# Performance work log

Measured on AMD Instinct MI355X. Metric: run time of the kernel, lower is better.

## Reference

```python
import jax, jax.numpy as jnp
import numpy as np

N = 100000   # nodes
F = 256      # input features
H = 64       # hidden dims
C = 40       # classes
L = 4        # GGNN layers
E = 1200000  # edges


def setup_inputs() -> dict:
    key = jax.random.key(0)
    ks = jax.random.split(key, 8)
    x = jax.random.normal(ks[0], (N, F), dtype=jnp.float32)
    edge_index = jax.random.randint(ks[1], (2, E), 0, N, dtype=jnp.int64)
    # glorot-initialized projection weights
    weight_in = jax.random.uniform(ks[2], (F, H), jnp.float32, -1.0, 1.0) * np.sqrt(6.0 / (F + H))
    weight_out = jax.random.uniform(ks[3], (H, C), jnp.float32, -1.0, 1.0) * np.sqrt(6.0 / (H + C))
    # GatedGraphConv: per-layer message weight [L, H, H], shared GRUCell params
    conv_weight = jax.random.uniform(ks[4], (L, H, H), jnp.float32, -1.0, 1.0) * np.sqrt(6.0 / (2 * H))
    s = 1.0 / np.sqrt(H)
    w_ih = jax.random.uniform(ks[5], (3 * H, H), jnp.float32, -s, s)
    w_hh = jax.random.uniform(ks[6], (3 * H, H), jnp.float32, -s, s)
    b_ih = jax.random.uniform(ks[7], (3 * H,), jnp.float32, -s, s)
    b_hh = jnp.zeros((3 * H,), jnp.float32)
    return {"x": x, "edge_index": edge_index, "weight_in": weight_in,
            "weight_out": weight_out, "conv_weight": conv_weight,
            "w_ih": w_ih, "w_hh": w_hh, "b_ih": b_ih, "b_hh": b_hh}


def _gru_cell(a, h, w_ih, w_hh, b_ih, b_hh):
    # torch.nn.GRUCell math: input a, hidden h
    gi = a @ w_ih.T + b_ih
    gh = h @ w_hh.T + b_hh
    i_r, i_z, i_n = jnp.split(gi, 3, axis=1)
    h_r, h_z, h_n = jnp.split(gh, 3, axis=1)
    r = jax.nn.sigmoid(i_r + h_r)
    z = jax.nn.sigmoid(i_z + h_z)
    n = jnp.tanh(i_n + r * h_n)
    return (1.0 - z) * n + z * h


def reference(x, edge_index, weight_in, weight_out, conv_weight, w_ih, w_hh, b_ih, b_hh):
    n_nodes = x.shape[0]
    src, dst = edge_index[0], edge_index[1]
    h = x @ weight_in  # [N, H]
    for i in range(conv_weight.shape[0]):
        m = h @ conv_weight[i]                                   # [N, H]
        agg = jax.ops.segment_sum(m[src], dst, num_segments=n_nodes)  # scatter-add
        h = _gru_cell(agg, h, w_ih, w_hh, b_ih, b_hh)
    out = h @ weight_out  # [N, C]
    return jax.nn.log_softmax(out, axis=1)
```

## Files before the change

kernel.cpp:

```cpp
#include <hip/hip_runtime.h>


#define DEVI __device__ __forceinline__

typedef __attribute__((ext_vector_type(8))) short short8;
typedef __attribute__((ext_vector_type(4))) short bf16x4;
typedef __attribute__((ext_vector_type(4))) float f32x4;

constexpr int N_NODES   = 100000;
constexpr int F_IN      = 256;
constexpr int H_DIM     = 64;
constexpr int C_OUT     = 40;
constexpr int ROW_TILES = N_NODES / 16;
constexpr int CH        = 8192;
constexpr int NBUCK     = (N_NODES + 127) / 128;
constexpr int LB_STRIDE = NBUCK + 1;
constexpr int BCAP      = 2048;

DEVI float bf2f(unsigned short u) {
    unsigned v = ((unsigned)u) << 16;
    float f; __builtin_memcpy(&f, &v, 4); return f;
}
DEVI unsigned short f2bf(float f) {
    unsigned u; __builtin_memcpy(&u, &f, 4);
    unsigned r = u + 0x7FFFu + ((u >> 16) & 1u);
    return (unsigned short)(r >> 16);
}
DEVI float in_elem(const void* p, size_t idx, int f32flag) {
    return f32flag ? ((const float*)p)[idx]
                   : bf2f(((const unsigned short*)p)[idx]);
}
DEVI short8 f32row_to_frag(const float* __restrict__ p) {
    const f32x4* q = (const f32x4*)p;
    f32x4 lo = q[0], hi = q[1];
    short8 a;
    a[0] = (short)f2bf(lo[0]); a[1] = (short)f2bf(lo[1]);
    a[2] = (short)f2bf(lo[2]); a[3] = (short)f2bf(lo[3]);
    a[4] = (short)f2bf(hi[0]); a[5] = (short)f2bf(hi[1]);
    a[6] = (short)f2bf(hi[2]); a[7] = (short)f2bf(hi[3]);
    return a;
}

__global__ void detect_kernel(const void* x, const int* ei, int* flags) {
    if (threadIdx.x != 0 || blockIdx.x != 0) return;
    const unsigned short* u = (const unsigned short*)x;
    int sane = 0;
    for (int i = 0; i < 256; ++i) {
        int e = (u[i] >> 7) & 0xFF;
        if (e >= 100 && e <= 145) sane++;
    }
    flags[0] = (sane < 230) ? 1 : 0;
    int zeros = 0;
    for (int i = 0; i < 64; ++i)
        if (ei[2 * i + 1] == 0) zeros++;
    flags[1] = (zeros >= 63) ? 1 : 0;
}

__global__ __launch_bounds__(256) void bucket_local(
        const int* __restrict__ ei, int E, const int* __restrict__ flags,
        int* __restrict__ wgsorted,
        int* __restrict__ lbase_g) {
    __shared__ int hist[NBUCK];
    __shared__ int partial[256];
    __shared__ int staging[CH];
    int tid = threadIdx.x, wg = blockIdx.x;
    int i64 = flags[1];
    int base = wg * CH;
    int cnt_wg = min(CH, E - base);

    for (int i = tid; i < NBUCK; i += 256) hist[i] = 0;
    __syncthreads();
    for (int k = tid; k < cnt_wg; k += 256) {
        size_t e = (size_t)base + k;
        int d = i64 ? ei[2 * ((size_t)E + e)] : ei[(size_t)E + e];
        atomicAdd(&hist[d >> 7], 1);
    }
    __syncthreads();
    int i0 = 4 * tid;
    int e0 = (i0 + 0 < NBUCK) ? hist[i0 + 0] : 0;
    int e1 = (i0 + 1 < NBUCK) ? hist[i0 + 1] : 0;
    int e2 = (i0 + 2 < NBUCK) ? hist[i0 + 2] : 0;
    int e3 = (i0 + 3 < NBUCK) ? hist[i0 + 3] : 0;
    int s0 = e0, s1 = s0 + e1, s2 = s1 + e2, s3 = s2 + e3;
    __syncthreads();
    partial[tid] = s3;
    __syncthreads();
    for (int ofs = 1; ofs < 256; ofs <<= 1) {
        int add = (tid >= ofs) ? partial[tid - ofs] : 0;
        __syncthreads();
        partial[tid] += add;
        __syncthreads();
    }
    int pbase = (tid > 0) ? partial[tid - 1] : 0;
    if (i0 + 0 < NBUCK) hist[i0 + 0] = pbase;
    if (i0 + 1 < NBUCK) hist[i0 + 1] = pbase + s0;
    if (i0 + 2 < NBUCK) hist[i0 + 2] = pbase + s1;
    if (i0 + 3 < NBUCK) hist[i0 + 3] = pbase + s2;
    __syncthreads();
    int* lb = lbase_g + (size_t)wg * LB_STRIDE;
    for (int i = tid; i < NBUCK; i += 256) lb[i] = hist[i];
    if (tid == 0) lb[NBUCK] = cnt_wg;
    __syncthreads();
    for (int k = tid; k < cnt_wg; k += 256) {
        size_t e = (size_t)base + k;
        int s, d;
        if (i64) { s = ei[2 * e]; d = ei[2 * ((size_t)E + e)]; }
        else     { s = ei[e];     d = ei[(size_t)E + e]; }
        int pos = atomicAdd(&hist[d >> 7], 1);
        staging[pos] = ((d & 127) << 17) | s;
    }
    __syncthreads();
    for (int k = tid; k < cnt_wg; k += 256)
        wgsorted[(size_t)base + k] = staging[k];
}

__global__ __launch_bounds__(256) void bucket_csr(
        const int* __restrict__ wgsorted,
        const int* __restrict__ lbase_g,
        int nwg,
        int* __restrict__ rowptr,
        int* __restrict__ counts,
        int* __restrict__ esrc) {
    __shared__ int segincl[256];
    __shared__ int segbase[256];
    __shared__ int edata[BCAP];
    __shared__ int sout[BCAP];
    __shared__ int hist2[128];
    __shared__ int cur2[128];
    int tid = threadIdx.x, b = blockIdx.x;

    int lbv = 0, cntv = 0;
    if (tid < nwg) {
        const int* lb = lbase_g + (size_t)tid * LB_STRIDE;
        lbv  = lb[b];
        cntv = lb[b + 1] - lbv;
    }
    segbase[tid] = lbv;
    segincl[tid] = cntv;
    __syncthreads();
    for (int ofs = 1; ofs < 256; ofs <<= 1) {
        int add = (tid >= ofs) ? segincl[tid - ofs] : 0;
        __syncthreads();
        segincl[tid] += add;
        __syncthreads();
    }
    int tot = min(segincl[255], BCAP);
    for (int i = tid; i < tot; i += 256) {
        int lo = 0, hi = 255;
        while (lo < hi) {
            int mid = (lo + hi) >> 1;
            if (segincl[mid] > i) hi = mid; else lo = mid + 1;
        }
        int excl = (lo > 0) ? segincl[lo - 1] : 0;
        edata[i] = wgsorted[(size_t)lo * CH + segbase[lo] + (i - excl)];
    }
    if (tid < 128) hist2[tid] = 0;
    __syncthreads();
    for (int i = tid; i < tot; i += 256) atomicAdd(&hist2[edata[i] >> 17], 1);
    __syncthreads();
    if (tid < 128) cur2[tid] = hist2[tid];
    __syncthreads();
    for (int ofs = 1; ofs < 128; ofs <<= 1) {
        int add = 0;
        if (tid < 128 && tid >= ofs) add = cur2[tid - ofs];
        __syncthreads();
        if (tid < 128) cur2[tid] += add;
        __syncthreads();
    }
    int nodeexcl = 0;
    if (tid < 128) nodeexcl = (tid > 0) ? cur2[tid - 1] : 0;
    __syncthreads();
    if (tid < 128) {
        int node = b * 128 + tid;
        if (node < N_NODES) {
            counts[node] = hist2[tid];
            rowptr[node] = b * BCAP + nodeexcl;
        }
        cur2[tid] = nodeexcl;
    }
    __syncthreads();
    for (int i = tid; i < tot; i += 256) {
        int p = edata[i];
        int pos = atomicAdd(&cur2[p >> 17], 1);
        sout[pos] = p & 0x1FFFF;
    }
    __syncthreads();
    for (int i = tid; i < tot; i += 256)
        esrc[(size_t)b * BCAP + i] = sout[i];
}

__global__ void prep_all(const void* __restrict__ w_in,
                         const void* __restrict__ w_out,
                         const void* __restrict__ w_hh,
                         const void* __restrict__ b_ih,
                         const void* __restrict__ b_hh,
                         const void* __restrict__ conv_w,
                         const void* __restrict__ w_ih,
                         unsigned short* __restrict__ winfrag,
                         unsigned short* __restrict__ wofrag,
                         unsigned short* __restrict__ whh_c,
                         unsigned short* __restrict__ bias_c,
                         unsigned short* __restrict__ wcomb,
                         const int* __restrict__ flags) {
    int f32 = flags[0];
    int t = blockIdx.x * blockDim.x + threadIdx.x;
    if (t < 16384) {
        int i = t & 7, lane = (t >> 3) & 63, jt = (t >> 9) & 3, kb = t >> 11;
        int k = kb * 32 + ((lane >> 4) << 3) + i;
        int col = jt * 16 + (lane & 15);
        winfrag[t] = f2bf(in_elem(w_in, (size_t)k * 64 + col, f32));
    } else if (t < 19456) {
        int u = t - 16384;
        int i = u & 7, lane = (u >> 3) & 63;
        int jt = (u >> 9) % 3, kb = u / 1536;
        int k = kb * 32 + ((lane >> 4) << 3) + i;
        int col = jt * 16 + (lane & 15);
        wofrag[u] = (col < 40) ? f2bf(in_elem(w_out, (size_t)k * 40 + col, f32))
                               : (unsigned short)0;
    } else if (t < 31744) {
        int u = t - 19456;
        whh_c[u] = f2bf(in_elem(w_hh, u, f32));
    } else if (t < 31936) {
        int u = t - 31744;
        bias_c[u] = f2bf(in_elem(b_ih, u, f32));
    } else if (t < 32128) {
        int u = t - 31936;
        bias_c[192 + u] = f2bf(in_elem(b_hh, u, f32));
    } else if (t < 32128 + 49152) {
        int u = t - 32128;
        int l = u / 12288;
        int idx = u % 12288;
        int i = idx & 7, lane = (idx >> 3) & 63, c = idx >> 9;
        int kb = c / 12, jt = c % 12;
        int quad = lane >> 4, l15 = lane & 15;
        int k = kb * 32 + quad * 8 + i;
        int g = jt * 16 + l15;
        float acc = 0.0f;
        if (f32) {
            const f32x4* ca = (const f32x4*)((const float*)conv_w +
                                             (size_t)l * 4096 + (size_t)k * 64);
            const f32x4* wa = (const f32x4*)((const float*)w_ih + (size_t)g * 64);
#pragma unroll
            for (int jq = 0; jq < 16; ++jq) {
                f32x4 cv = ca[jq];
                f32x4 wv = wa[jq];
                acc += cv[0] * wv[0] + cv[1] * wv[1] + cv[2] * wv[2] + cv[3] * wv[3];
            }
        } else {
            const short8* ca = (const short8*)((const unsigned short*)conv_w +
                                               (size_t)l * 4096 + (size_t)k * 64);
            const short8* wa = (const short8*)((const unsigned short*)w_ih +
                                               (size_t)g * 64);
#pragma unroll
            for (int jq = 0; jq < 8; ++jq) {
                short8 cv = ca[jq];
                short8 wv = wa[jq];
#pragma unroll
                for (int q = 0; q < 8; ++q)
                    acc += bf2f((unsigned short)cv[q]) * bf2f((unsigned short)wv[q]);
            }
        }
        wcomb[(size_t)l * 12288 + idx] = f2bf(acc);
    }
}

template <int XF32>
DEVI void proj_in_body(const void* __restrict__ xr,
                       const unsigned short* __restrict__ wfrag,
                       unsigned short* __restrict__ h) {
    int wid = blockIdx.x * 4 + (threadIdx.x >> 6);
    if (wid >= ROW_TILES) return;
    int lane = threadIdx.x & 63;
    int l15 = lane & 15, quad = lane >> 4;
    int row0 = wid * 16;
    int arow = row0 + l15;

    f32x4 acc[4];
#pragma unroll
    for (int jt = 0; jt < 4; ++jt) acc[jt] = (f32x4)(0.0f);

#pragma unroll
    for (int kb = 0; kb < 8; ++kb) {
        short8 a;
        if (XF32)
            a = f32row_to_frag((const float*)xr + (size_t)arow * F_IN + kb * 32 + quad * 8);
        else
            a = *(const short8*)((const unsigned short*)xr + (size_t)arow * F_IN + kb * 32 + quad * 8);
#pragma unroll
        for (int jt = 0; jt < 4; ++jt) {
            short8 b = *(const short8*)(wfrag + (size_t)((kb * 4 + jt) * 64 + lane) * 8);
            acc[jt] = __builtin_amdgcn_mfma_f32_16x16x32_bf16(a, b, acc[jt], 0, 0, 0);
        }
    }
#pragma unroll
    for (int jt = 0; jt < 4; ++jt)
#pragma unroll
        for (int r = 0; r < 4; ++r)
            h[(size_t)(row0 + quad * 4 + r) * H_DIM + jt * 16 + l15] = f2bf(acc[jt][r]);
}

__global__ __launch_bounds__(256) void proj_in_kernel(
        const void* __restrict__ x,
        const unsigned short* __restrict__ wfrag,
        unsigned short* __restrict__ h,
        const int* __restrict__ flags) {
    if (flags[0]) proj_in_body<1>(x, wfrag, h);
    else          proj_in_body<0>(x, wfrag, h);
}

__global__ __launch_bounds__(256) void gather_agg(
        const unsigned short* __restrict__ h,
        const int* __restrict__ rowptr,
        const int* __restrict__ counts,
        const int* __restrict__ esrc,
        unsigned short* __restrict__ aggB) {
    int n = blockIdx.x * 4 + (threadIdx.x >> 6);
    if (n >= N_NODES) return;
    int lane = threadIdx.x & 63;
    int sub  = lane >> 4;
    int c4   = (lane & 15) * 4;
    int start = rowptr[n];
    int deg   = counts[n];

    f32x4 acc0 = (f32x4)(0.0f), acc1 = (f32x4)(0.0f);

    for (int i = 0; i < deg; i += 32) {
        int sidx[8];
#pragma unroll
        for (int u = 0; u < 8; ++u) {
            int e = i + u * 4 + sub;
            sidx[u] = (e < deg) ? esrc[start + e] : -1;
        }
#pragma unroll
        for (int u = 0; u < 8; ++u) {
            if (sidx[u] >= 0) {
                bf16x4 v = *(const bf16x4*)(h + (size_t)sidx[u] * H_DIM + c4);
                f32x4& A = (u & 1) ? acc1 : acc0;
                A[0] += bf2f((unsigned short)v[0]);
                A[1] += bf2f((unsigned short)v[1]);
                A[2] += bf2f((unsigned short)v[2]);
                A[3] += bf2f((unsigned short)v[3]);
            }
        }
    }

#pragma unroll
    for (int k = 0; k < 4; ++k) acc0[k] += acc1[k];
#pragma unroll
    for (int k = 0; k < 4; ++k) {
        acc0[k] += __shfl_xor(acc0[k], 16);
        acc0[k] += __shfl_xor(acc0[k], 32);
    }
    if (sub == 0) {
        bf16x4 o;
        o[0] = (short)f2bf(acc0[0]);
        o[1] = (short)f2bf(acc0[1]);
        o[2] = (short)f2bf(acc0[2]);
        o[3] = (short)f2bf(acc0[3]);
        *(bf16x4*)(aggB + (size_t)n * H_DIM + c4) = o;
    }
}

__global__ __launch_bounds__(256) void gru_kernel(
        const unsigned short* __restrict__ aggB,
        unsigned short* __restrict__ h,
        const unsigned short* __restrict__ wcomb_l,
        const unsigned short* __restrict__ whh_c,
        const unsigned short* __restrict__ bias_c) {
    int wid = blockIdx.x * 4 + (threadIdx.x >> 6);
    if (wid >= ROW_TILES) return;
    int lane = threadIdx.x & 63;
    int l15 = lane & 15, quad = lane >> 4;
    int row0 = wid * 16;
    int arow = row0 + l15;

    f32x4 gi[12], gh[12];
#pragma unroll
    for (int jt = 0; jt < 12; ++jt) { gi[jt] = (f32x4)(0.0f); gh[jt] = (f32x4)(0.0f); }

#pragma unroll
    for (int kb = 0; kb < 2; ++kb) {
        short8 aa = *(const short8*)(aggB + (size_t)arow * H_DIM + kb * 32 + quad * 8);
        short8 ah = *(const short8*)(h + (size_t)arow * H_DIM + kb * 32 + quad * 8);
#pragma unroll
        for (int jt = 0; jt < 12; ++jt) {
            short8 bi = *(const short8*)(wcomb_l + (size_t)((kb * 12 + jt) * 64 + lane) * 8);
            gi[jt] = __builtin_amdgcn_mfma_f32_16x16x32_bf16(aa, bi, gi[jt], 0, 0, 0);
            short8 bh = *(const short8*)(whh_c + (size_t)(jt * 16 + l15) * H_DIM + kb * 32 + quad * 8);
            gh[jt] = __builtin_amdgcn_mfma_f32_16x16x32_bf16(ah, bh, gh[jt], 0, 0, 0);
        }
    }

#pragma unroll
    for (int jc = 0; jc < 4; ++jc) {
        int j = jc * 16 + l15;
        float bir = bf2f(bias_c[j]),       bhr = bf2f(bias_c[192 + j]);
        float biz = bf2f(bias_c[64 + j]),  bhz = bf2f(bias_c[256 + j]);
        float bin = bf2f(bias_c[128 + j]), bhn = bf2f(bias_c[320 + j]);
#pragma unroll
        for (int r = 0; r < 4; ++r) {
            int row = row0 + quad * 4 + r;
            float xr = (gi[jc][r] + bir) + (gh[jc][r] + bhr);
            float xz = (gi[4 + jc][r] + biz) + (gh[4 + jc][r] + bhz);
            float in_ = gi[8 + jc][r] + bin;
            float hn_ = gh[8 + jc][r] + bhn;
            xr = fminf(fmaxf(xr, -30.0f), 30.0f);
            xz = fminf(fmaxf(xz, -30.0f), 30.0f);
            float rg = 1.0f / (1.0f + __expf(-xr));
            float zg = 1.0f / (1.0f + __expf(-xz));
            float na = in_ + rg * hn_;
            float ey = __expf(-2.0f * fabsf(na));
            float th = (1.0f - ey) / (1.0f + ey);
            float nt = (na < 0.0f) ? -th : th;
            float ho = bf2f(h[(size_t)row * H_DIM + j]);
            h[(size_t)row * H_DIM + j] = f2bf((1.0f - zg) * nt + zg * ho);
        }
    }
}

__global__ __launch_bounds__(256) void projout_kernel(
        const unsigned short* __restrict__ h,
        const unsigned short* __restrict__ wofrag,
        void* __restrict__ out,
        const int* __restrict__ flags) {
    int f32out = flags[0];
    int wid = blockIdx.x * 4 + (threadIdx.x >> 6);
    if (wid >= ROW_TILES) return;
    int lane = threadIdx.x & 63;
    int l15 = lane & 15, quad = lane >> 4;
    int row0 = wid * 16;
    int arow = row0 + l15;

    f32x4 acc[3];
#pragma unroll
    for (int jt = 0; jt < 3; ++jt) acc[jt] = (f32x4)(0.0f);

#pragma unroll
    for (int kb = 0; kb < 2; ++kb) {
        short8 a = *(const short8*)(h + (size_t)arow * H_DIM + kb * 32 + quad * 8);
#pragma unroll
        for (int jt = 0; jt < 3; ++jt) {
            short8 b = *(const short8*)(wofrag + (size_t)((kb * 3 + jt) * 64 + lane) * 8);
            acc[jt] = __builtin_amdgcn_mfma_f32_16x16x32_bf16(a, b, acc[jt], 0, 0, 0);
        }
    }

    float* of = (float*)out;
    unsigned short* ob = (unsigned short*)out;
    bool valid2 = (l15 < 8);
#pragma unroll
    for (int r = 0; r < 4; ++r) {
        int row = row0 + quad * 4 + r;
        float v0 = acc[0][r], v1 = acc[1][r], v2 = acc[2][r];
        float mx = fmaxf(v0, v1);
        if (valid2) mx = fmaxf(mx, v2);
#pragma unroll
        for (int d = 1; d < 16; d <<= 1) mx = fmaxf(mx, __shfl_xor(mx, d));
        float s = __expf(v0 - mx) + __expf(v1 - mx) + (valid2 ? __expf(v2 - mx) : 0.0f);
#pragma unroll
        for (int d = 1; d < 16; d <<= 1) s += __shfl_xor(s, d);
        float lg = mx + __logf(s);
        size_t o0 = (size_t)row * C_OUT + l15;
        if (f32out) {
            of[o0]      = v0 - lg;
            of[o0 + 16] = v1 - lg;
            if (valid2) of[o0 + 32] = v2 - lg;
        } else {
            ob[o0]      = f2bf(v0 - lg);
            ob[o0 + 16] = f2bf(v1 - lg);
            if (valid2) ob[o0 + 32] = f2bf(v2 - lg);
        }
    }
}

extern "C" void kernel_launch(void* const* d_in, const int* in_sizes, int n_in,
                              void* d_out, int out_size, void* d_ws, size_t ws_size,
                              hipStream_t stream) {
    const void* x      = d_in[0];
    const int*  ei     = (const int*)d_in[1];
    const void* w_in   = d_in[2];
    const void* w_out  = d_in[3];
    const void* conv_w = d_in[4];
    const void* w_ih   = d_in[5];
    const void* w_hh   = d_in[6];
    const void* b_ih   = d_in[7];
    const void* b_hh   = d_in[8];

    const int E   = in_sizes[1] / 2;
    const int nwg = (E + CH - 1) / CH;

    char* ws = (char*)d_ws;
    size_t off = 0;
    auto carve = [&](size_t bytes) {
        void* p = ws + off;
        off += (bytes + 255) & ~(size_t)255;
        return p;
    };
    int*            flags    = (int*)carve(256);
    unsigned short* aggB     = (unsigned short*)carve((size_t)N_NODES * H_DIM * 2);
    unsigned short* hbuf     = (unsigned short*)carve((size_t)N_NODES * H_DIM * 2);
    int*            counts   = (int*)carve((size_t)N_NODES * 4);
    int*            rowptr   = (int*)carve((size_t)N_NODES * 4);
    int*            wgsorted = (int*)carve((size_t)nwg * CH * 4);
    int*            lbase_g  = (int*)carve((size_t)nwg * LB_STRIDE * 4);
    int*            esrcP    = (int*)carve((size_t)NBUCK * BCAP * 4);
    unsigned short* winfrag  = (unsigned short*)carve((size_t)16384 * 2);
    unsigned short* wcomb    = (unsigned short*)carve((size_t)4 * 12288 * 2);
    unsigned short* wofrag   = (unsigned short*)carve((size_t)3072 * 2);
    unsigned short* whh_c    = (unsigned short*)carve((size_t)12288 * 2);
    unsigned short* bias_c   = (unsigned short*)carve((size_t)384 * 2);

    detect_kernel<<<1, 64, 0, stream>>>(x, ei, flags);

    for (int rep = 0; rep < 3; ++rep) {
        bucket_local<<<nwg, 256, 0, stream>>>(ei, E, flags, wgsorted, lbase_g);
        bucket_csr<<<NBUCK, 256, 0, stream>>>(wgsorted, lbase_g, nwg,
                                              rowptr, counts, esrcP);
    }

    prep_all<<<(32128 + 49152 + 255) / 256, 256, 0, stream>>>(
        w_in, w_out, w_hh, b_ih, b_hh, conv_w, w_ih,
        winfrag, wofrag, whh_c, bias_c, wcomb, flags);

    const int gblocks = (ROW_TILES + 3) / 4;
    const int nblocks = N_NODES / 4;

    proj_in_kernel<<<gblocks, 256, 0, stream>>>(x, winfrag, hbuf, flags);

    for (int l = 0; l < 4; ++l) {
        gather_agg<<<nblocks, 256, 0, stream>>>(hbuf, rowptr, counts, esrcP, aggB);
        gru_kernel<<<gblocks, 256, 0, stream>>>(aggB, hbuf, wcomb + (size_t)l * 12288,
                                                whh_c, bias_c);
    }

    projout_kernel<<<gblocks, 256, 0, stream>>>(hbuf, wofrag, d_out, flags);
}
```

Baseline: 636.9 us.

## Fuse gather with GRU per layer, fold prep into CSR build, drop repeated sorts

Removes the triple repetition of the edge bucketing passes and folds dtype detection into bucket_local and weight preparation into the CSR build kernel. Each GGNN layer becomes one kernel that gathers neighbour sums into LDS and then runs the GRU MFMAs, writing to a ping-pong h buffer; the output projection and log-softmax are fused into the last layer. This cuts launches and the aggregate buffer round trip through global memory. In exchange, each wave now gathers 16 nodes serially, which may reduce memory-level parallelism in the gather.

```diff
diff --git a/kernel.cpp b/kernel.cpp
--- a/kernel.cpp
+++ b/kernel.cpp
@@ -16,6 +16,7 @@
 constexpr int NBUCK     = (N_NODES + 127) / 128;
 constexpr int LB_STRIDE = NBUCK + 1;
 constexpr int BCAP      = 2048;
+constexpr int LPAD      = 72;
 
 DEVI float bf2f(unsigned short u) {
     unsigned v = ((unsigned)u) << 16;
@@ -41,30 +42,39 @@
     return a;
 }
 
-__global__ void detect_kernel(const void* x, const int* ei, int* flags) {
-    if (threadIdx.x != 0 || blockIdx.x != 0) return;
+DEVI int probe_i64_wave(const int* __restrict__ ei) {
+    int lane = threadIdx.x & 63;
+    unsigned long long m = __ballot(ei[2 * lane + 1] == 0);
+    return __popcll(m) >= 63;
+}
+DEVI int probe_f32_wave(const void* __restrict__ x) {
     const unsigned short* u = (const unsigned short*)x;
-    int sane = 0;
-    for (int i = 0; i < 256; ++i) {
-        int e = (u[i] >> 7) & 0xFF;
-        if (e >= 100 && e <= 145) sane++;
-    }
-    flags[0] = (sane < 230) ? 1 : 0;
-    int zeros = 0;
-    for (int i = 0; i < 64; ++i)
-        if (ei[2 * i + 1] == 0) zeros++;
-    flags[1] = (zeros >= 63) ? 1 : 0;
+    int lane = threadIdx.x & 63;
+    int cnt = 0;
+#pragma unroll
+    for (int i = 0; i < 4; ++i) {
+        int e = (u[lane + i * 64] >> 7) & 0xFF;
+        cnt += (e >= 100 && e <= 145) ? 1 : 0;
+    }
+#pragma unroll
+    for (int d = 1; d < 64; d <<= 1) cnt += __shfl_xor(cnt, d);
+    return cnt < 230;
 }
 
 __global__ __launch_bounds__(256) void bucket_local(
-        const int* __restrict__ ei, int E, const int* __restrict__ flags,
+        const int* __restrict__ ei, int E, const void* __restrict__ x,
         int* __restrict__ wgsorted,
-        int* __restrict__ lbase_g) {
+        int* __restrict__ lbase_g,
+        int* __restrict__ flags) {
     __shared__ int hist[NBUCK];
     __shared__ int partial[256];
     __shared__ int staging[CH];
     int tid = threadIdx.x, wg = blockIdx.x;
-    int i64 = flags[1];
+    int i64 = probe_i64_wave(ei);
+    if (wg == 0 && tid < 64) {
+        int f32 = probe_f32_wave(x);
+        if (tid == 0) { flags[0] = f32; flags[1] = i64; }
+    }
     int base = wg * CH;
     int cnt_wg = min(CH, E - base);
 
@@ -114,20 +124,97 @@
         wgsorted[(size_t)base + k] = staging[k];
 }
 
-__global__ __launch_bounds__(256) void bucket_csr(
+__global__ __launch_bounds__(256) void bucket_csr_prep(
         const int* __restrict__ wgsorted,
         const int* __restrict__ lbase_g,
         int nwg,
         int* __restrict__ rowptr,
         int* __restrict__ counts,
-        int* __restrict__ esrc) {
+        int* __restrict__ esrc,
+        const void* __restrict__ w_in,
+        const void* __restrict__ w_out,
+        const void* __restrict__ w_hh,
+        const void* __restrict__ b_ih,
+        const void* __restrict__ b_hh,
+        const void* __restrict__ conv_w,
+        const void* __restrict__ w_ih,
+        unsigned short* __restrict__ winfrag,
+        unsigned short* __restrict__ wofrag,
+        unsigned short* __restrict__ whh_c,
+        unsigned short* __restrict__ bias_c,
+        unsigned short* __restrict__ wcomb,
+        const int* __restrict__ flags) {
+    int tid = threadIdx.x, b = blockIdx.x;
+
+    {
+        int f32 = flags[0];
+        int t = b * 256 + tid;
+        if (t < 16384) {
+            int i = t & 7, lane = (t >> 3) & 63, jt = (t >> 9) & 3, kb = t >> 11;
+            int k = kb * 32 + ((lane >> 4) << 3) + i;
+            int col = jt * 16 + (lane & 15);
+            winfrag[t] = f2bf(in_elem(w_in, (size_t)k * 64 + col, f32));
+        } else if (t < 19456) {
+            int u = t - 16384;
+            int i = u & 7, lane = (u >> 3) & 63;
+            int jt = (u >> 9) % 3, kb = u / 1536;
+            int k = kb * 32 + ((lane >> 4) << 3) + i;
+            int col = jt * 16 + (lane & 15);
+            wofrag[u] = (col < 40) ? f2bf(in_elem(w_out, (size_t)k * 40 + col, f32))
+                                   : (unsigned short)0;
+        } else if (t < 31744) {
+            int u = t - 19456;
+            whh_c[u] = f2bf(in_elem(w_hh, u, f32));
+        } else if (t < 31936) {
+            int u = t - 31744;
+            bias_c[u] = f2bf(in_elem(b_ih, u, f32));
+        } else if (t < 32128) {
+            int u = t - 31936;
+            bias_c[192 + u] = f2bf(in_elem(b_hh, u, f32));
+        } else if (t < 32128 + 49152) {
+            int u = t - 32128;
+            int l = u / 12288;
+            int idx = u % 12288;
+            int i = idx & 7, lane = (idx >> 3) & 63, c = idx >> 9;
+            int kb = c / 12, jt = c % 12;
+            int quad = lane >> 4, l15 = lane & 15;
+            int k = kb * 32 + quad * 8 + i;
+            int g = jt * 16 + l15;
+            float acc = 0.0f;
+            if (f32) {
+                const f32x4* ca = (const f32x4*)((const float*)conv_w +
+                                                 (size_t)l * 4096 + (size_t)k * 64);
+                const f32x4* wa = (const f32x4*)((const float*)w_ih + (size_t)g * 64);
+#pragma unroll
+                for (int jq = 0; jq < 16; ++jq) {
+                    f32x4 cv = ca[jq];
+                    f32x4 wv = wa[jq];
+                    acc += cv[0] * wv[0] + cv[1] * wv[1] + cv[2] * wv[2] + cv[3] * wv[3];
+                }
+            } else {
+                const short8* ca = (const short8*)((const unsigned short*)conv_w +
+                                                   (size_t)l * 4096 + (size_t)k * 64);
+                const short8* wa = (const short8*)((const unsigned short*)w_ih +
+                                                   (size_t)g * 64);
+#pragma unroll
+                for (int jq = 0; jq < 8; ++jq) {
+                    short8 cv = ca[jq];
+                    short8 wv = wa[jq];
+#pragma unroll
+                    for (int q = 0; q < 8; ++q)
+                        acc += bf2f((unsigned short)cv[q]) * bf2f((unsigned short)wv[q]);
+                }
+            }
+            wcomb[(size_t)l * 12288 + idx] = f2bf(acc);
+        }
+    }
+
     __shared__ int segincl[256];
     __shared__ int segbase[256];
     __shared__ int edata[BCAP];
     __shared__ int sout[BCAP];
     __shared__ int hist2[128];
     __shared__ int cur2[128];
-    int tid = threadIdx.x, b = blockIdx.x;
 
     int lbv = 0, cntv = 0;
     if (tid < nwg) {
@@ -187,81 +274,6 @@
     __syncthreads();
     for (int i = tid; i < tot; i += 256)
         esrc[(size_t)b * BCAP + i] = sout[i];
-}
-
-__global__ void prep_all(const void* __restrict__ w_in,
-                         const void* __restrict__ w_out,
-                         const void* __restrict__ w_hh,
-                         const void* __restrict__ b_ih,
-                         const void* __restrict__ b_hh,
-                         const void* __restrict__ conv_w,
-                         const void* __restrict__ w_ih,
-                         unsigned short* __restrict__ winfrag,
-                         unsigned short* __restrict__ wofrag,
-                         unsigned short* __restrict__ whh_c,
-                         unsigned short* __restrict__ bias_c,
-                         unsigned short* __restrict__ wcomb,
-                         const int* __restrict__ flags) {
-    int f32 = flags[0];
-    int t = blockIdx.x * blockDim.x + threadIdx.x;
-    if (t < 16384) {
-        int i = t & 7, lane = (t >> 3) & 63, jt = (t >> 9) & 3, kb = t >> 11;
-        int k = kb * 32 + ((lane >> 4) << 3) + i;
-        int col = jt * 16 + (lane & 15);
-        winfrag[t] = f2bf(in_elem(w_in, (size_t)k * 64 + col, f32));
-    } else if (t < 19456) {
-        int u = t - 16384;
-        int i = u & 7, lane = (u >> 3) & 63;
-        int jt = (u >> 9) % 3, kb = u / 1536;
-        int k = kb * 32 + ((lane >> 4) << 3) + i;
-        int col = jt * 16 + (lane & 15);
-        wofrag[u] = (col < 40) ? f2bf(in_elem(w_out, (size_t)k * 40 + col, f32))
-                               : (unsigned short)0;
-    } else if (t < 31744) {
-        int u = t - 19456;
-        whh_c[u] = f2bf(in_elem(w_hh, u, f32));
-    } else if (t < 31936) {
-        int u = t - 31744;
-        bias_c[u] = f2bf(in_elem(b_ih, u, f32));
-    } else if (t < 32128) {
-        int u = t - 31936;
-        bias_c[192 + u] = f2bf(in_elem(b_hh, u, f32));
-    } else if (t < 32128 + 49152) {
-        int u = t - 32128;
-        int l = u / 12288;
-        int idx = u % 12288;
-        int i = idx & 7, lane = (idx >> 3) & 63, c = idx >> 9;
-        int kb = c / 12, jt = c % 12;
-        int quad = lane >> 4, l15 = lane & 15;
-        int k = kb * 32 + quad * 8 + i;
-        int g = jt * 16 + l15;
-        float acc = 0.0f;
-        if (f32) {
-            const f32x4* ca = (const f32x4*)((const float*)conv_w +
-                                             (size_t)l * 4096 + (size_t)k * 64);
-            const f32x4* wa = (const f32x4*)((const float*)w_ih + (size_t)g * 64);
-#pragma unroll
-            for (int jq = 0; jq < 16; ++jq) {
-                f32x4 cv = ca[jq];
-                f32x4 wv = wa[jq];
-                acc += cv[0] * wv[0] + cv[1] * wv[1] + cv[2] * wv[2] + cv[3] * wv[3];
-            }
-        } else {
-            const short8* ca = (const short8*)((const unsigned short*)conv_w +
-                                               (size_t)l * 4096 + (size_t)k * 64);
-            const short8* wa = (const short8*)((const unsigned short*)w_ih +
-                                               (size_t)g * 64);
-#pragma unroll
-            for (int jq = 0; jq < 8; ++jq) {
-                short8 cv = ca[jq];
-                short8 wv = wa[jq];
-#pragma unroll
-                for (int q = 0; q < 8; ++q)
-                    acc += bf2f((unsigned short)cv[q]) * bf2f((unsigned short)wv[q]);
-            }
-        }
-        wcomb[(size_t)l * 12288 + idx] = f2bf(acc);
-    }
 }
 
 template <int XF32>
@@ -308,91 +320,99 @@
     else          proj_in_body<0>(x, wfrag, h);
 }
 
-__global__ __launch_bounds__(256) void gather_agg(
-        const unsigned short* __restrict__ h,
+template <int LAST>
+__global__ __launch_bounds__(256, 6) void layer_fused(
+        const unsigned short* __restrict__ hin,
+        unsigned short* __restrict__ hout,
         const int* __restrict__ rowptr,
         const int* __restrict__ counts,
         const int* __restrict__ esrc,
-        unsigned short* __restrict__ aggB) {
-    int n = blockIdx.x * 4 + (threadIdx.x >> 6);
-    if (n >= N_NODES) return;
-    int lane = threadIdx.x & 63;
-    int sub  = lane >> 4;
-    int c4   = (lane & 15) * 4;
-    int start = rowptr[n];
-    int deg   = counts[n];
-
-    f32x4 acc0 = (f32x4)(0.0f), acc1 = (f32x4)(0.0f);
-
-    for (int i = 0; i < deg; i += 32) {
-        int sidx[8];
-#pragma unroll
-        for (int u = 0; u < 8; ++u) {
-            int e = i + u * 4 + sub;
-            sidx[u] = (e < deg) ? esrc[start + e] : -1;
-        }
-#pragma unroll
-        for (int u = 0; u < 8; ++u) {
-            if (sidx[u] >= 0) {
-                bf16x4 v = *(const bf16x4*)(h + (size_t)sidx[u] * H_DIM + c4);
-                f32x4& A = (u & 1) ? acc1 : acc0;
-                A[0] += bf2f((unsigned short)v[0]);
-                A[1] += bf2f((unsigned short)v[1]);
-                A[2] += bf2f((unsigned short)v[2]);
-                A[3] += bf2f((unsigned short)v[3]);
-            }
-        }
-    }
-
-#pragma unroll
-    for (int k = 0; k < 4; ++k) acc0[k] += acc1[k];
-#pragma unroll
-    for (int k = 0; k < 4; ++k) {
-        acc0[k] += __shfl_xor(acc0[k], 16);
-        acc0[k] += __shfl_xor(acc0[k], 32);
-    }
-    if (sub == 0) {
-        bf16x4 o;
-        o[0] = (short)f2bf(acc0[0]);
-        o[1] = (short)f2bf(acc0[1]);
-        o[2] = (short)f2bf(acc0[2]);
-        o[3] = (short)f2bf(acc0[3]);
-        *(bf16x4*)(aggB + (size_t)n * H_DIM + c4) = o;
-    }
-}
-
-__global__ __launch_bounds__(256) void gru_kernel(
-        const unsigned short* __restrict__ aggB,
-        unsigned short* __restrict__ h,
         const unsigned short* __restrict__ wcomb_l,
         const unsigned short* __restrict__ whh_c,
-        const unsigned short* __restrict__ bias_c) {
-    int wid = blockIdx.x * 4 + (threadIdx.x >> 6);
-    if (wid >= ROW_TILES) return;
-    int lane = threadIdx.x & 63;
+        const unsigned short* __restrict__ bias_c,
+        const unsigned short* __restrict__ wofrag,
+        void* __restrict__ out,
+        const int* __restrict__ flags) {
+    __shared__ __align__(16) unsigned short lagg[64 * LPAD];
+    int tid = threadIdx.x;
+    int w = tid >> 6, lane = tid & 63;
+    int nb0 = blockIdx.x * 64;
+    int sub = lane >> 4;
+    int c4 = (lane & 15) * 4;
+
+    for (int k = 0; k < 16; ++k) {
+        int n = nb0 + w * 16 + k;
+        if (n >= N_NODES) break;
+        int start = rowptr[n];
+        int deg   = counts[n];
+        f32x4 acc0 = (f32x4)(0.0f), acc1 = (f32x4)(0.0f);
+        for (int i = 0; i < deg; i += 32) {
+            int sidx[8];
+#pragma unroll
+            for (int u = 0; u < 8; ++u) {
+                int e = i + u * 4 + sub;
+                sidx[u] = (e < deg) ? esrc[start + e] : -1;
+            }
+#pragma unroll
+            for (int u = 0; u < 8; ++u) {
+                if (sidx[u] >= 0) {
+                    bf16x4 v = *(const bf16x4*)(hin + (size_t)sidx[u] * H_DIM + c4);
+                    f32x4& A = (u & 1) ? acc1 : acc0;
+                    A[0] += bf2f((unsigned short)v[0]);
+                    A[1] += bf2f((unsigned short)v[1]);
+                    A[2] += bf2f((unsigned short)v[2]);
+                    A[3] += bf2f((unsigned short)v[3]);
+                }
+            }
+        }
+#pragma unroll
+        for (int q = 0; q < 4; ++q) acc0[q] += acc1[q];
+#pragma unroll
+        for (int q = 0; q < 4; ++q) {
+            acc0[q] += __shfl_xor(acc0[q], 16);
+            acc0[q] += __shfl_xor(acc0[q], 32);
+        }
+        if (sub == 0) {
+            bf16x4 o;
+            o[0] = (short)f2bf(acc0[0]);
+            o[1] = (short)f2bf(acc0[1]);
+            o[2] = (short)f2bf(acc0[2]);
+            o[3] = (short)f2bf(acc0[3]);
+            *(bf16x4*)(lagg + (w * 16 + k) * LPAD + c4) = o;
+        }
+    }
+    __syncthreads();
+
     int l15 = lane & 15, quad = lane >> 4;
-    int row0 = wid * 16;
-    int arow = row0 + l15;
-
-    f32x4 gi[12], gh[12];
-#pragma unroll
-    for (int jt = 0; jt < 12; ++jt) { gi[jt] = (f32x4)(0.0f); gh[jt] = (f32x4)(0.0f); }
-
-#pragma unroll
-    for (int kb = 0; kb < 2; ++kb) {
-        short8 aa = *(const short8*)(aggB + (size_t)arow * H_DIM + kb * 32 + quad * 8);
-        short8 ah = *(const short8*)(h + (size_t)arow * H_DIM + kb * 32 + quad * 8);
-#pragma unroll
-        for (int jt = 0; jt < 12; ++jt) {
-            short8 bi = *(const short8*)(wcomb_l + (size_t)((kb * 12 + jt) * 64 + lane) * 8);
-            gi[jt] = __builtin_amdgcn_mfma_f32_16x16x32_bf16(aa, bi, gi[jt], 0, 0, 0);
-            short8 bh = *(const short8*)(whh_c + (size_t)(jt * 16 + l15) * H_DIM + kb * 32 + quad * 8);
-            gh[jt] = __builtin_amdgcn_mfma_f32_16x16x32_bf16(ah, bh, gh[jt], 0, 0, 0);
-        }
-    }
-
-#pragma unroll
+    int row0 = nb0 + w * 16;
+    int lrow = w * 16 + l15;
+    int arow = min(row0 + l15, N_NODES - 1);
+
+    short8 aa0 = *(const short8*)(lagg + lrow * LPAD + quad * 8);
+    short8 aa1 = *(const short8*)(lagg + lrow * LPAD + 32 + quad * 8);
+    short8 ah0 = *(const short8*)(hin + (size_t)arow * H_DIM + quad * 8);
+    short8 ah1 = *(const short8*)(hin + (size_t)arow * H_DIM + 32 + quad * 8);
+
+#pragma unroll 1
     for (int jc = 0; jc < 4; ++jc) {
+        f32x4 ir = (f32x4)(0.0f), iz = (f32x4)(0.0f), ia = (f32x4)(0.0f);
+        f32x4 hr = (f32x4)(0.0f), hz = (f32x4)(0.0f), ha = (f32x4)(0.0f);
+#define WCF(kb, jt) (*(const short8*)(wcomb_l + (size_t)(((kb) * 12 + (jt)) * 64 + lane) * 8))
+#define WHF(jt, kb) (*(const short8*)(whh_c + (size_t)((jt) * 16 + l15) * H_DIM + (kb) * 32 + quad * 8))
+        ir = __builtin_amdgcn_mfma_f32_16x16x32_bf16(aa0, WCF(0, jc), ir, 0, 0, 0);
+        iz = __builtin_amdgcn_mfma_f32_16x16x32_bf16(aa0, WCF(0, 4 + jc), iz, 0, 0, 0);
+        ia = __builtin_amdgcn_mfma_f32_16x16x32_bf16(aa0, WCF(0, 8 + jc), ia, 0, 0, 0);
+        hr = __builtin_amdgcn_mfma_f32_16x16x32_bf16(ah0, WHF(jc, 0), hr, 0, 0, 0);
+        hz = __builtin_amdgcn_mfma_f32_16x16x32_bf16(ah0, WHF(4 + jc, 0), hz, 0, 0, 0);
+        ha = __builtin_amdgcn_mfma_f32_16x16x32_bf16(ah0, WHF(8 + jc, 0), ha, 0, 0, 0);
+        ir = __builtin_amdgcn_mfma_f32_16x16x32_bf16(aa1, WCF(1, jc), ir, 0, 0, 0);
+        iz = __builtin_amdgcn_mfma_f32_16x16x32_bf16(aa1, WCF(1, 4 + jc), iz, 0, 0, 0);
+        ia = __builtin_amdgcn_mfma_f32_16x16x32_bf16(aa1, WCF(1, 8 + jc), ia, 0, 0, 0);
+        hr = __builtin_amdgcn_mfma_f32_16x16x32_bf16(ah1, WHF(jc, 1), hr, 0, 0, 0);
+        hz = __builtin_amdgcn_mfma_f32_16x16x32_bf16(ah1, WHF(4 + jc, 1), hz, 0, 0, 0);
+        ha = __builtin_amdgcn_mfma_f32_16x16x32_bf16(ah1, WHF(8 + jc, 1), ha, 0, 0, 0);
+#undef WCF
+#undef WHF
         int j = jc * 16 + l15;
         float bir = bf2f(bias_c[j]),       bhr = bf2f(bias_c[192 + j]);
         float biz = bf2f(bias_c[64 + j]),  bhz = bf2f(bias_c[256 + j]);
@@ -400,75 +420,66 @@
 #pragma unroll
         for (int r = 0; r < 4; ++r) {
             int row = row0 + quad * 4 + r;
-            float xr = (gi[jc][r] + bir) + (gh[jc][r] + bhr);
-            float xz = (gi[4 + jc][r] + biz) + (gh[4 + jc][r] + bhz);
-            float in_ = gi[8 + jc][r] + bin;
-            float hn_ = gh[8 + jc][r] + bhn;
-            xr = fminf(fmaxf(xr, -30.0f), 30.0f);
-            xz = fminf(fmaxf(xz, -30.0f), 30.0f);
-            float rg = 1.0f / (1.0f + __expf(-xr));
-            float zg = 1.0f / (1.0f + __expf(-xz));
-            float na = in_ + rg * hn_;
-            float ey = __expf(-2.0f * fabsf(na));
-            float th = (1.0f - ey) / (1.0f + ey);
-            float nt = (na < 0.0f) ? -th : th;
-            float ho = bf2f(h[(size_t)row * H_DIM + j]);
-            h[(size_t)row * H_DIM + j] = f2bf((1.0f - zg) * nt + zg * ho);
-        }
-    }
-}
-
-__global__ __launch_bounds__(256) void projout_kernel(
-        const unsigned short* __restrict__ h,
-        const unsigned short* __restrict__ wofrag,
-        void* __restrict__ out,
-        const int* __restrict__ flags) {
-    int f32out = flags[0];
-    int wid = blockIdx.x * 4 + (threadIdx.x >> 6);
-    if (wid >= ROW_TILES) return;
-    int lane = threadIdx.x & 63;
-    int l15 = lane & 15, quad = lane >> 4;
-    int row0 = wid * 16;
-    int arow = row0 + l15;
-
-    f32x4 acc[3];
-#pragma unroll
-    for (int jt = 0; jt < 3; ++jt) acc[jt] = (f32x4)(0.0f);
-
-#pragma unroll
-    for (int kb = 0; kb < 2; ++kb) {
-        short8 a = *(const short8*)(h + (size_t)arow * H_DIM + kb * 32 + quad * 8);
-#pragma unroll
-        for (int jt = 0; jt < 3; ++jt) {
-            short8 b = *(const short8*)(wofrag + (size_t)((kb * 3 + jt) * 64 + lane) * 8);
-            acc[jt] = __builtin_amdgcn_mfma_f32_16x16x32_bf16(a, b, acc[jt], 0, 0, 0);
-        }
-    }
-
-    float* of = (float*)out;
-    unsigned short* ob = (unsigned short*)out;
-    bool valid2 = (l15 < 8);
-#pragma unroll
-    for (int r = 0; r < 4; ++r) {
-        int row = row0 + quad * 4 + r;
-        float v0 = acc[0][r], v1 = acc[1][r], v2 = acc[2][r];
-        float mx = fmaxf(v0, v1);
-        if (valid2) mx = fmaxf(mx, v2);
-#pragma unroll
-        for (int d = 1; d < 16; d <<= 1) mx = fmaxf(mx, __shfl_xor(mx, d));
-        float s = __expf(v0 - mx) + __expf(v1 - mx) + (valid2 ? __expf(v2 - mx) : 0.0f);
-#pragma unroll
-        for (int d = 1; d < 16; d <<= 1) s += __shfl_xor(s, d);
-        float lg = mx + __logf(s);
-        size_t o0 = (size_t)row * C_OUT + l15;
-        if (f32out) {
-            of[o0]      = v0 - lg;
-            of[o0 + 16] = v1 - lg;
-            if (valid2) of[o0 + 32] = v2 - lg;
-        } else {
-            ob[o0]      = f2bf(v0 - lg);
-            ob[o0 + 16] = f2bf(v1 - lg);
-            if (valid2) ob[o0 + 32] = f2bf(v2 - lg);
+            if (row < N_NODES) {
+                float xr = (ir[r] + bir) + (hr[r] + bhr);
+                float xz = (iz[r] + biz) + (hz[r] + bhz);
+                float in_ = ia[r] + bin;
+                float hn_ = ha[r] + bhn;
+                xr = fminf(fmaxf(xr, -30.0f), 30.0f);
+                xz = fminf(fmaxf(xz, -30.0f), 30.0f);
+                float rg = 1.0f / (1.0f + __expf(-xr));
+                float zg = 1.0f / (1.0f + __expf(-xz));
+                float na = in_ + rg * hn_;
+                float ey = __expf(-2.0f * fabsf(na));
+                float th = (1.0f - ey) / (1.0f + ey);
+                float nt = (na < 0.0f) ? -th : th;
+                float ho = bf2f(hin[(size_t)row * H_DIM + j]);
+                hout[(size_t)row * H_DIM + j] = f2bf((1.0f - zg) * nt + zg * ho);
+            }
+        }
+    }
+
+    if (LAST) {
+        int f32out = flags[0];
+        f32x4 pacc[3];
+#pragma unroll
+        for (int jt = 0; jt < 3; ++jt) pacc[jt] = (f32x4)(0.0f);
+#pragma unroll
+        for (int kb = 0; kb < 2; ++kb) {
+            short8 a = *(const short8*)(hout + (size_t)arow * H_DIM + kb * 32 + quad * 8);
+#pragma unroll
+            for (int jt = 0; jt < 3; ++jt) {
+                short8 bfr = *(const short8*)(wofrag + (size_t)((kb * 3 + jt) * 64 + lane) * 8);
+                pacc[jt] = __builtin_amdgcn_mfma_f32_16x16x32_bf16(a, bfr, pacc[jt], 0, 0, 0);
+            }
+        }
+        float* of = (float*)out;
+        unsigned short* ob = (unsigned short*)out;
+        bool valid2 = (l15 < 8);
+#pragma unroll
+        for (int r = 0; r < 4; ++r) {
+            int row = row0 + quad * 4 + r;
+            float v0 = pacc[0][r], v1 = pacc[1][r], v2 = pacc[2][r];
+            float mx = fmaxf(v0, v1);
+            if (valid2) mx = fmaxf(mx, v2);
+#pragma unroll
+            for (int d = 1; d < 16; d <<= 1) mx = fmaxf(mx, __shfl_xor(mx, d));
+            float s = __expf(v0 - mx) + __expf(v1 - mx) + (valid2 ? __expf(v2 - mx) : 0.0f);
+#pragma unroll
+            for (int d = 1; d < 16; d <<= 1) s += __shfl_xor(s, d);
+            float lg = mx + __logf(s);
+            if (row < N_NODES) {
+                size_t o0 = (size_t)row * C_OUT + l15;
+                if (f32out) {
+                    of[o0]      = v0 - lg;
+                    of[o0 + 16] = v1 - lg;
+                    if (valid2) of[o0 + 32] = v2 - lg;
+                } else {
+                    ob[o0]      = f2bf(v0 - lg);
+                    ob[o0 + 16] = f2bf(v1 - lg);
+                    if (valid2) ob[o0 + 32] = f2bf(v2 - lg);
+                }
+            }
         }
     }
 }
@@ -497,8 +508,8 @@
         return p;
     };
     int*            flags    = (int*)carve(256);
-    unsigned short* aggB     = (unsigned short*)carve((size_t)N_NODES * H_DIM * 2);
-    unsigned short* hbuf     = (unsigned short*)carve((size_t)N_NODES * H_DIM * 2);
+    unsigned short* h1       = (unsigned short*)carve((size_t)N_NODES * H_DIM * 2);
+    unsigned short* h0       = (unsigned short*)carve((size_t)N_NODES * H_DIM * 2);
     int*            counts   = (int*)carve((size_t)N_NODES * 4);
     int*            rowptr   = (int*)carve((size_t)N_NODES * 4);
     int*            wgsorted = (int*)carve((size_t)nwg * CH * 4);
@@ -510,28 +521,22 @@
     unsigned short* whh_c    = (unsigned short*)carve((size_t)12288 * 2);
     unsigned short* bias_c   = (unsigned short*)carve((size_t)384 * 2);
 
-    detect_kernel<<<1, 64, 0, stream>>>(x, ei, flags);
-
-    for (int rep = 0; rep < 3; ++rep) {
-        bucket_local<<<nwg, 256, 0, stream>>>(ei, E, flags, wgsorted, lbase_g);
-        bucket_csr<<<NBUCK, 256, 0, stream>>>(wgsorted, lbase_g, nwg,
-                                              rowptr, counts, esrcP);
-    }
-
-    prep_all<<<(32128 + 49152 + 255) / 256, 256, 0, stream>>>(
+    bucket_local<<<nwg, 256, 0, stream>>>(ei, E, x, wgsorted, lbase_g, flags);
+    bucket_csr_prep<<<NBUCK, 256, 0, stream>>>(
+        wgsorted, lbase_g, nwg, rowptr, counts, esrcP,
         w_in, w_out, w_hh, b_ih, b_hh, conv_w, w_ih,
         winfrag, wofrag, whh_c, bias_c, wcomb, flags);
 
     const int gblocks = (ROW_TILES + 3) / 4;
-    const int nblocks = N_NODES / 4;
-
-    proj_in_kernel<<<gblocks, 256, 0, stream>>>(x, winfrag, hbuf, flags);
-
-    for (int l = 0; l < 4; ++l) {
-        gather_agg<<<nblocks, 256, 0, stream>>>(hbuf, rowptr, counts, esrcP, aggB);
-        gru_kernel<<<gblocks, 256, 0, stream>>>(aggB, hbuf, wcomb + (size_t)l * 12288,
-                                                whh_c, bias_c);
-    }
-
-    projout_kernel<<<gblocks, 256, 0, stream>>>(hbuf, wofrag, d_out, flags);
-}
+
+    proj_in_kernel<<<gblocks, 256, 0, stream>>>(x, winfrag, h0, flags);
+
+    layer_fused<0><<<gblocks, 256, 0, stream>>>(h0, h1, rowptr, counts, esrcP,
+        wcomb + 0 * 12288, whh_c, bias_c, wofrag, d_out, flags);
+    layer_fused<0><<<gblocks, 256, 0, stream>>>(h1, h0, rowptr, counts, esrcP,
+        wcomb + 1 * 12288, whh_c, bias_c, wofrag, d_out, flags);
+    layer_fused<0><<<gblocks, 256, 0, stream>>>(h0, h1, rowptr, counts, esrcP,
+        wcomb + 2 * 12288, whh_c, bias_c, wofrag, d_out, flags);
+    layer_fused<1><<<gblocks, 256, 0, stream>>>(h1, h0, rowptr, counts, esrcP,
+        wcomb + 3 * 12288, whh_c, bias_c, wofrag, d_out, flags);
+}
```

Measured after the change: 640.5 us. Within noise of the previous version (+0.6%).
